# Kernel optimization log

Hardware: AMD Instinct MI355X
Metric: run time of the kernel (lower is better)

## Reference

```python
import jax, jax.numpy as jnp
import numpy as np

KS = 7
HEADS = 8


def _conv1x1(a, w, b):
    # a: (B,Cin,H,W), w: (Cout,Cin), b: (Cout,)
    return jnp.einsum('bchw,oc->bohw', a, w) + b[None, :, None, None]


def _unfold2d(a, ks):
    # a: (B,C,Hp,Wp) -> (B,C,H,W,ks,ks) sliding windows, stride 1
    H = a.shape[2] - ks + 1
    W = a.shape[3] - ks + 1
    ii = jnp.arange(H)[:, None] + jnp.arange(ks)[None, :]  # (H,ks)
    jj = jnp.arange(W)[:, None] + jnp.arange(ks)[None, :]  # (W,ks)
    return a[:, :, ii[:, None, :, None], jj[None, :, None, :]]


def setup_inputs() -> dict:
    key = jax.random.key(0)
    ks = jax.random.split(key, 10)
    B, C, H, W = 4, 128, 56, 56
    x = jax.random.normal(ks[0], (B, C, H, W), dtype=jnp.float32)
    sc = 1.0 / np.sqrt(C)
    q_w = jax.random.normal(ks[1], (C, C), dtype=jnp.float32) * sc
    q_b = jax.random.normal(ks[2], (C,), dtype=jnp.float32) * 0.01
    k_w = jax.random.normal(ks[3], (C, C), dtype=jnp.float32) * sc
    k_b = jax.random.normal(ks[4], (C,), dtype=jnp.float32) * 0.01
    v_w = jax.random.normal(ks[5], (C, C), dtype=jnp.float32) * sc
    v_b = jax.random.normal(ks[6], (C,), dtype=jnp.float32) * 0.01
    rel_h = jax.random.normal(ks[7], (C // 2, KS, 1), dtype=jnp.float32)
    rel_w = jax.random.normal(ks[8], (C // 2, 1, KS), dtype=jnp.float32)
    return {'x': x, 'q_w': q_w, 'q_b': q_b, 'k_w': k_w, 'k_b': k_b,
            'v_w': v_w, 'v_b': v_b, 'rel_h': rel_h, 'rel_w': rel_w}


def reference(x, q_w, q_b, k_w, k_b, v_w, v_b, rel_h, rel_w):
    B, C, H, W = x.shape
    dkh = C // HEADS
    K2 = KS * KS
    pl = (KS - 1) // 2
    pr = KS - 1 - pl
    xp = jnp.pad(x, ((0, 0), (0, 0), (pl, pr), (pl, pr)))

    k = _conv1x1(xp, k_w, k_b)
    v = _conv1x1(xp, v_w, v_b)
    q = _conv1x1(x, q_w, q_b)

    # unfold K/V into (B,C,H,W,KS,KS) then reshape exactly as torch does
    # (this reshape intermixes channel/window axes; replicated faithfully)
    k6 = _unfold2d(k, KS).reshape(B, HEADS, H, W, dkh, K2)
    v6 = _unfold2d(v, KS).reshape(B, HEADS, H, W, dkh, K2)
    q6 = q.reshape(B, HEADS, H, W, dkh, 1)

    # q^T k over the dkh axis -> (B,heads,H,W,KS,KS)
    qk = jnp.einsum('bhxyd,bhxydk->bhxyk', q6[..., 0], k6)
    qk = qk.reshape(B, HEADS, H, W, KS, KS)

    # einsum 'bhxydz,cij->bhxyij' has no shared index: factorizes as
    # (sum over d,z of q) * (sum over c of rel)
    qsum = q6.sum(axis=(4, 5))  # (B,heads,H,W)
    qk = qk + qsum[..., None, None] * rel_h.sum(axis=0)  # (KS,1) broadcast
    qk = qk + qsum[..., None, None] * rel_w.sum(axis=0)  # (1,KS) broadcast

    w = jax.nn.softmax(qk.reshape(B, HEADS, H, W, K2), axis=-1)
    out = jnp.einsum('bhxyk,bhxydk->bhxyd', w, v6)  # (B,heads,H,W,dvh)
    return out.reshape(B, C, H, W)
```

## Files before the change

kernel.cpp:

```cpp
#include <hip/hip_runtime.h>
#include <hip/hip_bf16.h>
#include <math.h>

#define NB    4
#define NC    128
#define NPIX  3136
#define CHW   401408
#define SKS   68
#define STS   19

template <int CTRL, int RM>
__device__ __forceinline__ float dpp_mov(float x, float old) {
    return __int_as_float(__builtin_amdgcn_update_dpp(
        __float_as_int(old), __float_as_int(x), CTRL, RM, 0xf, false));
}
__device__ __forceinline__ float wave_sum(float x) {
    x = x + dpp_mov<0x111, 0xf>(x, 0.f);
    x = x + dpp_mov<0x112, 0xf>(x, 0.f);
    x = x + dpp_mov<0x114, 0xf>(x, 0.f);
    x = x + dpp_mov<0x118, 0xf>(x, 0.f);
    x = x + dpp_mov<0x142, 0xa>(x, 0.f);
    x = x + dpp_mov<0x143, 0xc>(x, 0.f);
    return __int_as_float(__builtin_amdgcn_readlane(__float_as_int(x), 63));
}

__device__ __forceinline__ float qk16(const float* kp, const float* kp2,
                                      float4 r0, float4 r1, float4 r2, float4 r3) {
    float a0, a1;
    a0  = r0.x * kp[0];   a1  = r0.y * kp[1];
    a0 += r0.z * kp[2];   a1 += r0.w * kp[3];
    a0 += r1.x * kp[4];   a1 += r1.y * kp[5];
    a0 += r1.z * kp[6];   a1 += r1.w * kp[7];
    a0 += r2.x * kp2[0];  a1 += r2.y * kp2[1];
    a0 += r2.z * kp2[2];  a1 += r2.w * kp2[3];
    a0 += r3.x * kp2[4];  a1 += r3.y * kp2[5];
    a0 += r3.z * kp2[6];  a1 += r3.w * kp2[7];
    return a0 + a1;
}
__device__ __forceinline__ float sum16(float4 r0, float4 r1, float4 r2, float4 r3) {
    return (((r0.x + r0.y) + (r0.z + r0.w)) + ((r1.x + r1.y) + (r1.z + r1.w)))
         + (((r2.x + r2.y) + (r2.z + r2.w)) + ((r3.x + r3.y) + (r3.z + r3.w)));
}

__global__ __launch_bounds__(256) void prep_kernel(
    const float* __restrict__ qw, const float* __restrict__ kw,
    const float* __restrict__ vw,
    const float* __restrict__ rel_h, const float* __restrict__ rel_w,
    float* __restrict__ w4q, float* __restrict__ w4k, float* __restrict__ w4v,
    float* __restrict__ rb)
{
    int idx = blockIdx.x * 256 + threadIdx.x;
    if (idx < 3 * 16384) {
        int m = idx >> 14;
        int r = idx & 16383;
        int cc = r & 3;
        int t = r >> 2;
        int o = t & 127;
        int c4 = t >> 7;
        const float* src = (m == 0) ? qw : (m == 1) ? kw : vw;
        float* dst = (m == 0) ? w4q : (m == 1) ? w4k : w4v;
        dst[r] = src[o * 128 + c4 * 4 + cc];
    }
    if (idx < 14) {
        const float* src = (idx < 7) ? rel_h : rel_w;
        int off = (idx < 7) ? idx : idx - 7;
        float s = 0.f;
        for (int c = 0; c < 64; ++c) s += src[c * 7 + off];
        rb[idx] = s;
    }
}

__global__ __launch_bounds__(256) void conv_kernel(
    const float* __restrict__ x,
    const float* __restrict__ w4q, const float* __restrict__ w4k,
    const float* __restrict__ w4v,
    const float* __restrict__ qb, const float* __restrict__ kb,
    const float* __restrict__ vb,
    float* __restrict__ q, float* __restrict__ kbuf, float* __restrict__ vbuf)
{
    __shared__ float sx[128 * 16];
    __shared__ float st[3 * 128 * STS];
    int bid = blockIdx.x;
    int tile = bid % 196;
    int b = bid / 196;
    int pix0 = tile * 16;
    const float* xb = x + b * CHW + pix0;

    for (int i = threadIdx.x; i < 512; i += 256) {
        int c = i >> 2, p4 = (i & 3) * 4;
        *(float4*)(sx + c * 16 + p4) = *(const float4*)(xb + c * NPIX + p4);
    }
    __syncthreads();

    int lane = threadIdx.x & 63;
    int wave = threadIdx.x >> 6;
    int o = wave * 32 + (lane & 31);
    int ph = (lane >> 5) * 8;
    const float4* Wq = (const float4*)w4q + o;
    const float4* Wk = (const float4*)w4k + o;
    const float4* Wv = (const float4*)w4v + o;

    float4 wqc = Wq[0], wkc = Wk[0], wvc = Wv[0];
    float aq[8] = {}, ak[8] = {}, av[8] = {};
    #pragma unroll 1
    for (int c4 = 0; c4 < 32; ++c4) {
        float4 xs[8];
        #pragma unroll
        for (int cc = 0; cc < 4; ++cc) {
            xs[2 * cc]     = *(const float4*)(sx + (c4 * 4 + cc) * 16 + ph);
            xs[2 * cc + 1] = *(const float4*)(sx + (c4 * 4 + cc) * 16 + ph + 4);
        }
        float4 wq4 = wqc, wk4 = wkc, wv4 = wvc;
        if (c4 < 31) {
            wqc = Wq[(c4 + 1) * 128];
            wkc = Wk[(c4 + 1) * 128];
            wvc = Wv[(c4 + 1) * 128];
        }
        float wqr[4] = {wq4.x, wq4.y, wq4.z, wq4.w};
        float wkr[4] = {wk4.x, wk4.y, wk4.z, wk4.w};
        float wvr[4] = {wv4.x, wv4.y, wv4.z, wv4.w};
        #pragma unroll
        for (int cc = 0; cc < 4; ++cc) {
            float4 xa = xs[2 * cc], xc = xs[2 * cc + 1];
            float xv[8] = {xa.x, xa.y, xa.z, xa.w, xc.x, xc.y, xc.z, xc.w};
            #pragma unroll
            for (int p = 0; p < 8; ++p) {
                aq[p] += wqr[cc] * xv[p];
                ak[p] += wkr[cc] * xv[p];
                av[p] += wvr[cc] * xv[p];
            }
        }
    }
    float bq = qb[o], bk = kb[o], bv = vb[o];
    float* wrq = st + o * STS + ph;
    float* wrk = st + 128 * STS + o * STS + ph;
    float* wrv = st + 2 * 128 * STS + o * STS + ph;
    #pragma unroll
    for (int p = 0; p < 8; ++p) {
        wrq[p] = aq[p] + bq;
        wrk[p] = ak[p] + bk;
        wrv[p] = av[p] + bv;
    }
    __syncthreads();

    int pix = threadIdx.x & 15;
    int o8 = (threadIdx.x >> 4) * 8;
    float* qd = q + b * CHW + pix0 + pix;
    float* kd = kbuf + b * CHW + pix0 + pix;
    float* vd = vbuf + b * CHW + pix0 + pix;
    #pragma unroll
    for (int i = 0; i < 8; ++i) {
        int r = o8 + i;
        qd[r * NPIX] = st[r * STS + pix];
        kd[r * NPIX] = st[128 * STS + r * STS + pix];
        vd[r * NPIX] = st[2 * 128 * STS + r * STS + pix];
    }
}

__global__ __launch_bounds__(256) void attn_kernel(
    const float* __restrict__ q, const float* __restrict__ kbuf,
    const float* __restrict__ vbuf,
    const float* __restrict__ kb, const float* __restrict__ vb,
    const float* __restrict__ rb, float* __restrict__ out)
{
    __shared__ float sK[20 * SKS];
    __shared__ float sV[21 * SKS];
    __shared__ float sW[4 * 64];
    int bid = blockIdx.x;
    int qpart = bid & 3;
    int bc = bid >> 2;
    int ch = bc & 127;
    const float* qc = q + bc * NPIX + 784 * qpart;
    const float* kc = kbuf + bc * NPIX;
    const float* vc = vbuf + bc * NPIX;
    float* oc = out + bc * NPIX + 784 * qpart;
    float kbias = kb[ch], vbias = vb[ch];
    int qr0 = 14 * qpart;

    for (int i = threadIdx.x; i < 20 * 62; i += 256) {
        int yy = i / 62, xx = i - yy * 62;
        int gy = qr0 + yy - 3;
        int gx = xx - 3;
        bool in = (gy >= 0) && (gy < 56) && (gx >= 0) && (gx < 56);
        int off = in ? gy * 56 + gx : 0;
        float kv = in ? kc[off] : kbias;
        float vv = in ? vc[off] : vbias;
        sK[yy * SKS + xx] = kv;
        sV[yy * SKS + xx] = vv;
    }
    for (int i = threadIdx.x; i < SKS; i += 256) sV[20 * SKS + i] = 0.f;

    int lane = threadIdx.x & 63;
    int wave = threadIdx.x >> 6;
    int k2 = min(lane, 48);
    int di = k2 / 7, dj = k2 - di * 7;
    float rbias = rb[di] + rb[7 + dj];
    int koff = di * SKS + dj;
    int t16 = lane & 15, p = lane >> 4;
    float* sWw = sW + wave * 64;

    float rhM = rb[0], rhm = rb[0];
    #pragma unroll
    for (int i = 1; i < 7; ++i) { rhM = fmaxf(rhM, rb[i]); rhm = fminf(rhm, rb[i]); }
    float rwM = rb[7], rwm = rb[7];
    #pragma unroll
    for (int i = 8; i < 14; ++i) { rwM = fmaxf(rwM, rb[i]); rwm = fminf(rwm, rb[i]); }
    float rdMax = rbias - (rhM + rwM);
    float rdMin = rbias - (rhm + rwm);

    int ul0 = wave * 16;
    int y0 = 0, x0 = ul0;
    float4 p0 = *(const float4*)(qc + ul0);
    float4 p1 = *(const float4*)(qc + ul0 + 4);
    float4 p2 = *(const float4*)(qc + ul0 + 8);
    float4 p3 = *(const float4*)(qc + ul0 + 12);
    __syncthreads();

    for (int gl = wave; gl < 49; gl += 4) {
        float qs = sum16(p0, p1, p2, p3);
        const float* kp = sK + y0 * SKS + x0 + koff;
        int d2 = (x0 == 48) ? (SKS - 48) : 8;
        float acc = qk16(kp, kp + d2, p0, p1, p2, p3);

        if (gl + 4 < 49) {
            int un = ul0 + 64;
            p0 = *(const float4*)(qc + un);
            p1 = *(const float4*)(qc + un + 4);
            p2 = *(const float4*)(qc + un + 8);
            p3 = *(const float4*)(qc + un + 12);
        }

        float rd = (qs > 0.f) ? rdMax : rdMin;
        float ex = fmaf(qs, rd, acc);
        float e = (lane < 49) ? __expf(ex) : 0.f;
        float sS = wave_sum(e);
        float wgt = e * __builtin_amdgcn_rcpf(sS);
        sWw[lane] = wgt;

        int u = ul0 + t16;
        int yt = u / 56;
        int xt = u - yt * 56;
        const float* vbase = sV + yt * SKS + xt + p * (2 * SKS);
        const float* wbase = sWw + p * 14;
        float o0 = 0.f, o1 = 0.f;
        #pragma unroll
        for (int j = 0; j < 7; ++j) o0 += wbase[j] * vbase[j];
        #pragma unroll
        for (int j = 0; j < 7; ++j) o1 += wbase[7 + j] * vbase[SKS + j];
        float oacc = o0 + o1;
        oacc += __shfl_xor(oacc, 16);
        oacc += __shfl_xor(oacc, 32);
        if (lane < 16) oc[ul0 + lane] = oacc;

        ul0 += 64;
        x0 += 8; y0 += 1;
        if (x0 >= 56) { x0 -= 56; ++y0; }
    }
}

extern "C" void kernel_launch(void* const* d_in, const int* in_sizes, int n_in,
                              void* d_out, int out_size, void* d_ws, size_t ws_size,
                              hipStream_t stream) {
    const float* x     = (const float*)d_in[0];
    const float* qw    = (const float*)d_in[1];
    const float* qb    = (const float*)d_in[2];
    const float* kw    = (const float*)d_in[3];
    const float* kb    = (const float*)d_in[4];
    const float* vw    = (const float*)d_in[5];
    const float* vb    = (const float*)d_in[6];
    const float* rel_h = (const float*)d_in[7];
    const float* rel_w = (const float*)d_in[8];
    float* out = (float*)d_out;

    float* ws   = (float*)d_ws;
    float* kbuf = ws;
    float* vbuf = kbuf + 1605632;
    float* qbuf = vbuf + 1605632;
    float* w4q  = qbuf + 1605632;
    float* w4k  = w4q + 16384;
    float* w4v  = w4k + 16384;
    float* rb   = w4v + 16384;

    prep_kernel<<<192, 256, 0, stream>>>(qw, kw, vw, rel_h, rel_w,
                                         w4q, w4k, w4v, rb);
    conv_kernel<<<784, 256, 0, stream>>>(x, w4q, w4k, w4v, qb, kb, vb,
                                         qbuf, kbuf, vbuf);
    attn_kernel<<<2048, 256, 0, stream>>>(qbuf, kbuf, vbuf, kb, vb, rb, out);
}
```

Baseline: 70.04 us.

## Halve conv block size, compute two output channels per thread, reuse one staging buffer

The 1x1 conv kernel now runs with 128 threads per block, and each thread accumulates two output channels (o and o+64) for q, k and v, so every x value read from LDS feeds twice as many FMAs. The transpose staging buffer shrinks from three full tiles to one, reused for q, k and v in turn with extra barriers, which cuts LDS use per block. The attention helper functions are inlined by hand with no change to behaviour. The trade-offs are more registers per thread (48 accumulators), fewer waves per block and more barriers in the store phase.

```diff
diff --git a/kernel.cpp b/kernel.cpp
--- a/kernel.cpp
+++ b/kernel.cpp
@@ -7,7 +7,7 @@
 #define NPIX  3136
 #define CHW   401408
 #define SKS   68
-#define STS   19
+#define CTS   19
 
 template <int CTRL, int RM>
 __device__ __forceinline__ float dpp_mov(float x, float old) {
@@ -22,24 +22,6 @@
     x = x + dpp_mov<0x142, 0xa>(x, 0.f);
     x = x + dpp_mov<0x143, 0xc>(x, 0.f);
     return __int_as_float(__builtin_amdgcn_readlane(__float_as_int(x), 63));
-}
-
-__device__ __forceinline__ float qk16(const float* kp, const float* kp2,
-                                      float4 r0, float4 r1, float4 r2, float4 r3) {
-    float a0, a1;
-    a0  = r0.x * kp[0];   a1  = r0.y * kp[1];
-    a0 += r0.z * kp[2];   a1 += r0.w * kp[3];
-    a0 += r1.x * kp[4];   a1 += r1.y * kp[5];
-    a0 += r1.z * kp[6];   a1 += r1.w * kp[7];
-    a0 += r2.x * kp2[0];  a1 += r2.y * kp2[1];
-    a0 += r2.z * kp2[2];  a1 += r2.w * kp2[3];
-    a0 += r3.x * kp2[4];  a1 += r3.y * kp2[5];
-    a0 += r3.z * kp2[6];  a1 += r3.w * kp2[7];
-    return a0 + a1;
-}
-__device__ __forceinline__ float sum16(float4 r0, float4 r1, float4 r2, float4 r3) {
-    return (((r0.x + r0.y) + (r0.z + r0.w)) + ((r1.x + r1.y) + (r1.z + r1.w)))
-         + (((r2.x + r2.y) + (r2.z + r2.w)) + ((r3.x + r3.y) + (r3.z + r3.w)));
 }
 
 __global__ __launch_bounds__(256) void prep_kernel(
@@ -70,7 +52,7 @@
     }
 }
 
-__global__ __launch_bounds__(256) void conv_kernel(
+__global__ __launch_bounds__(128) void conv_kernel(
     const float* __restrict__ x,
     const float* __restrict__ w4q, const float* __restrict__ w4k,
     const float* __restrict__ w4v,
@@ -78,15 +60,15 @@
     const float* __restrict__ vb,
     float* __restrict__ q, float* __restrict__ kbuf, float* __restrict__ vbuf)
 {
-    __shared__ float sx[128 * 16];
-    __shared__ float st[3 * 128 * STS];
+    __shared__ float smem[128 * CTS];
+    float* sx = smem;
     int bid = blockIdx.x;
     int tile = bid % 196;
     int b = bid / 196;
     int pix0 = tile * 16;
     const float* xb = x + b * CHW + pix0;
 
-    for (int i = threadIdx.x; i < 512; i += 256) {
+    for (int i = threadIdx.x; i < 512; i += 128) {
         int c = i >> 2, p4 = (i & 3) * 4;
         *(float4*)(sx + c * 16 + p4) = *(const float4*)(xb + c * NPIX + p4);
     }
@@ -94,14 +76,17 @@
 
     int lane = threadIdx.x & 63;
     int wave = threadIdx.x >> 6;
-    int o = wave * 32 + (lane & 31);
+    int ob = wave * 32 + (lane & 31);
     int ph = (lane >> 5) * 8;
-    const float4* Wq = (const float4*)w4q + o;
-    const float4* Wk = (const float4*)w4k + o;
-    const float4* Wv = (const float4*)w4v + o;
-
-    float4 wqc = Wq[0], wkc = Wk[0], wvc = Wv[0];
-    float aq[8] = {}, ak[8] = {}, av[8] = {};
+    const float4* Wq = (const float4*)w4q;
+    const float4* Wk = (const float4*)w4k;
+    const float4* Wv = (const float4*)w4v;
+
+    float4 wqA = Wq[ob], wqB = Wq[ob + 64];
+    float4 wkA = Wk[ob], wkB = Wk[ob + 64];
+    float4 wvA = Wv[ob], wvB = Wv[ob + 64];
+    float aq0[8] = {}, aq1[8] = {}, ak0[8] = {}, ak1[8] = {};
+    float av0[8] = {}, av1[8] = {};
     #pragma unroll 1
     for (int c4 = 0; c4 < 32; ++c4) {
         float4 xs[8];
@@ -110,50 +95,75 @@
             xs[2 * cc]     = *(const float4*)(sx + (c4 * 4 + cc) * 16 + ph);
             xs[2 * cc + 1] = *(const float4*)(sx + (c4 * 4 + cc) * 16 + ph + 4);
         }
-        float4 wq4 = wqc, wk4 = wkc, wv4 = wvc;
+        float4 cqA = wqA, cqB = wqB, ckA = wkA, ckB = wkB, cvA = wvA, cvB = wvB;
         if (c4 < 31) {
-            wqc = Wq[(c4 + 1) * 128];
-            wkc = Wk[(c4 + 1) * 128];
-            wvc = Wv[(c4 + 1) * 128];
-        }
-        float wqr[4] = {wq4.x, wq4.y, wq4.z, wq4.w};
-        float wkr[4] = {wk4.x, wk4.y, wk4.z, wk4.w};
-        float wvr[4] = {wv4.x, wv4.y, wv4.z, wv4.w};
+            int nx = (c4 + 1) * 128;
+            wqA = Wq[nx + ob]; wqB = Wq[nx + ob + 64];
+            wkA = Wk[nx + ob]; wkB = Wk[nx + ob + 64];
+            wvA = Wv[nx + ob]; wvB = Wv[nx + ob + 64];
+        }
+        float qA[4] = {cqA.x, cqA.y, cqA.z, cqA.w};
+        float qB[4] = {cqB.x, cqB.y, cqB.z, cqB.w};
+        float kA[4] = {ckA.x, ckA.y, ckA.z, ckA.w};
+        float kB[4] = {ckB.x, ckB.y, ckB.z, ckB.w};
+        float vA[4] = {cvA.x, cvA.y, cvA.z, cvA.w};
+        float vB[4] = {cvB.x, cvB.y, cvB.z, cvB.w};
         #pragma unroll
         for (int cc = 0; cc < 4; ++cc) {
             float4 xa = xs[2 * cc], xc = xs[2 * cc + 1];
             float xv[8] = {xa.x, xa.y, xa.z, xa.w, xc.x, xc.y, xc.z, xc.w};
             #pragma unroll
             for (int p = 0; p < 8; ++p) {
-                aq[p] += wqr[cc] * xv[p];
-                ak[p] += wkr[cc] * xv[p];
-                av[p] += wvr[cc] * xv[p];
+                aq0[p] += qA[cc] * xv[p];  aq1[p] += qB[cc] * xv[p];
+                ak0[p] += kA[cc] * xv[p];  ak1[p] += kB[cc] * xv[p];
+                av0[p] += vA[cc] * xv[p];  av1[p] += vB[cc] * xv[p];
             }
         }
     }
-    float bq = qb[o], bk = kb[o], bv = vb[o];
-    float* wrq = st + o * STS + ph;
-    float* wrk = st + 128 * STS + o * STS + ph;
-    float* wrv = st + 2 * 128 * STS + o * STS + ph;
-    #pragma unroll
-    for (int p = 0; p < 8; ++p) {
-        wrq[p] = aq[p] + bq;
-        wrk[p] = ak[p] + bk;
-        wrv[p] = av[p] + bv;
-    }
-    __syncthreads();
+    float bq0 = qb[ob], bq1 = qb[ob + 64];
+    float bk0 = kb[ob], bk1 = kb[ob + 64];
+    float bv0 = vb[ob], bv1 = vb[ob + 64];
 
     int pix = threadIdx.x & 15;
-    int o8 = (threadIdx.x >> 4) * 8;
-    float* qd = q + b * CHW + pix0 + pix;
-    float* kd = kbuf + b * CHW + pix0 + pix;
-    float* vd = vbuf + b * CHW + pix0 + pix;
-    #pragma unroll
-    for (int i = 0; i < 8; ++i) {
-        int r = o8 + i;
-        qd[r * NPIX] = st[r * STS + pix];
-        kd[r * NPIX] = st[128 * STS + r * STS + pix];
-        vd[r * NPIX] = st[2 * 128 * STS + r * STS + pix];
+    int og = threadIdx.x >> 4;
+    float* wr0 = smem + ob * CTS + ph;
+    float* wr1 = smem + (ob + 64) * CTS + ph;
+
+    __syncthreads();
+    #pragma unroll
+    for (int p = 0; p < 8; ++p) { wr0[p] = aq0[p] + bq0; wr1[p] = aq1[p] + bq1; }
+    __syncthreads();
+    {
+        float* qd = q + b * CHW + pix0 + pix;
+        #pragma unroll
+        for (int i = 0; i < 16; ++i) {
+            int r = og * 16 + i;
+            qd[r * NPIX] = smem[r * CTS + pix];
+        }
+    }
+    __syncthreads();
+    #pragma unroll
+    for (int p = 0; p < 8; ++p) { wr0[p] = ak0[p] + bk0; wr1[p] = ak1[p] + bk1; }
+    __syncthreads();
+    {
+        float* kd = kbuf + b * CHW + pix0 + pix;
+        #pragma unroll
+        for (int i = 0; i < 16; ++i) {
+            int r = og * 16 + i;
+            kd[r * NPIX] = smem[r * CTS + pix];
+        }
+    }
+    __syncthreads();
+    #pragma unroll
+    for (int p = 0; p < 8; ++p) { wr0[p] = av0[p] + bv0; wr1[p] = av1[p] + bv1; }
+    __syncthreads();
+    {
+        float* vd = vbuf + b * CHW + pix0 + pix;
+        #pragma unroll
+        for (int i = 0; i < 16; ++i) {
+            int r = og * 16 + i;
+            vd[r * NPIX] = smem[r * CTS + pix];
+        }
     }
 }
 
@@ -217,10 +227,21 @@
     __syncthreads();
 
     for (int gl = wave; gl < 49; gl += 4) {
-        float qs = sum16(p0, p1, p2, p3);
+        float qs = (((p0.x + p0.y) + (p0.z + p0.w)) + ((p1.x + p1.y) + (p1.z + p1.w)))
+                 + (((p2.x + p2.y) + (p2.z + p2.w)) + ((p3.x + p3.y) + (p3.z + p3.w)));
         const float* kp = sK + y0 * SKS + x0 + koff;
         int d2 = (x0 == 48) ? (SKS - 48) : 8;
-        float acc = qk16(kp, kp + d2, p0, p1, p2, p3);
+        const float* kp2 = kp + d2;
+        float a0, a1;
+        a0  = p0.x * kp[0];   a1  = p0.y * kp[1];
+        a0 += p0.z * kp[2];   a1 += p0.w * kp[3];
+        a0 += p1.x * kp[4];   a1 += p1.y * kp[5];
+        a0 += p1.z * kp[6];   a1 += p1.w * kp[7];
+        a0 += p2.x * kp2[0];  a1 += p2.y * kp2[1];
+        a0 += p2.z * kp2[2];  a1 += p2.w * kp2[3];
+        a0 += p3.x * kp2[4];  a1 += p3.y * kp2[5];
+        a0 += p3.z * kp2[6];  a1 += p3.w * kp2[7];
+        float acc = a0 + a1;
 
         if (gl + 4 < 49) {
             int un = ul0 + 64;
@@ -283,7 +304,7 @@
 
     prep_kernel<<<192, 256, 0, stream>>>(qw, kw, vw, rel_h, rel_w,
                                          w4q, w4k, w4v, rb);
-    conv_kernel<<<784, 256, 0, stream>>>(x, w4q, w4k, w4v, qb, kb, vb,
+    conv_kernel<<<784, 128, 0, stream>>>(x, w4q, w4k, w4v, qb, kb, vb,
                                          qbuf, kbuf, vbuf);
     attn_kernel<<<2048, 256, 0, stream>>>(qbuf, kbuf, vbuf, kb, vb, rb, out);
 }
```

Result: slower. 79.51 us (+13.5%).
